# Kernel optimization log

Hardware: AMD Instinct MI355X
Metric: run time of the kernel (lower is better)

Reference implementation:

```python
import jax, jax.numpy as jnp
import numpy as np

EPS = 1e-5
INIT_PERSIST = 0.5

def _layernorm(x):
    mu = jnp.mean(x, axis=-1, keepdims=True)
    var = jnp.var(x, axis=-1, keepdims=True)
    return (x - mu) / jnp.sqrt(var + EPS)

def setup_inputs() -> dict:
    key = jax.random.key(0)
    k1, k2, k3, k4 = jax.random.split(key, 4)
    B, T, D, N = 8, 48, 512, 1024
    return {
        "x_seq": jax.random.normal(k1, (B, T, D), dtype=jnp.float32),
        "targets": jax.random.normal(k2, (B, T, D), dtype=jnp.float32),
        "E": jax.random.normal(k3, (D, N), dtype=jnp.float32) * 0.1,
        "Dy": jax.random.normal(k4, (N, D), dtype=jnp.float32) * 0.1,
        "mix_param": jnp.zeros((), dtype=jnp.float32),
    }

def reference(x_seq, targets, E, Dy, mix_param):
    B, T, D = x_seq.shape
    N = E.shape[1]
    alpha = jax.nn.sigmoid(mix_param)

    # initial states: persist = 0.5*I, transition = 0
    Gp0 = jnp.broadcast_to(jnp.eye(N, dtype=x_seq.dtype) * INIT_PERSIST, (B, N, N))
    Gt0 = jnp.zeros((B, N, N), dtype=x_seq.dtype)

    # target for step t's update is targets[:, t+1]; last step has no update
    tgt_next = jnp.concatenate([targets[:, 1:, :], jnp.zeros_like(targets[:, :1, :])], axis=1)
    do_upd = jnp.arange(T) < (T - 1)  # [T] bool

    xs = (jnp.swapaxes(x_seq, 0, 1), jnp.swapaxes(tgt_next, 0, 1), do_upd)

    def step(carry, inp):
        Gp, Gt = carry
        x_t, tn_t, upd = inp
        xn = jax.nn.relu(_layernorm(x_t @ E))          # [B, N]
        r_p = jnp.einsum("bn,bnm->bm", xn, Gp)
        r_t = jnp.einsum("bn,bnm->bm", xn, Gt)
        y = jax.nn.relu((alpha * r_p + (1.0 - alpha) * r_t) @ Dy)  # [B, D]
        tn = jax.nn.relu(_layernorm(tn_t @ E))          # [B, N]
        Gt_new = jnp.maximum(Gt, 0.5 * xn[:, :, None] * tn[:, None, :])
        Gp_new = jnp.maximum(Gp, 0.5 * xn[:, :, None] * xn[:, None, :])
        Gt = jnp.where(upd, Gt_new, Gt)
        Gp = jnp.where(upd, Gp_new, Gp)
        return (Gp, Gt), y

    _, ys = jax.lax.scan(step, (Gp0, Gt0), xs)
    return jnp.swapaxes(ys, 0, 1)  # [B, T, D]
```

## Files before the change

kernel.cpp:

```cpp
#include <hip/hip_runtime.h>
#include <math.h>

#define BB 8
#define TT 48
#define DD 512
#define NN 1024

__global__ __launch_bounds__(256) void k_gemm_z(const float* __restrict__ x,
                                                const float* __restrict__ tg,
                                                const float* __restrict__ E,
                                                float* __restrict__ z_x,
                                                float* __restrict__ z_t) {
    int rt = blockIdx.x, ct = blockIdx.y;
    int tid = threadIdx.x;
    int tr = tid >> 4;
    int tc = tid & 15;
    int row0 = rt * 32;
    int col0 = ct * 64;

    __shared__ float As[32][16];
    __shared__ float Es[16][64];

    int e2 = tid * 2;
    int sr = e2 >> 4;
    int sk0 = e2 & 15;
    int gr_s = row0 + sr;
    const float* srow;
    if (gr_s < BB * TT) {
        srow = x + (size_t)gr_s * DD;
    } else {
        int s = gr_s - BB * TT + 1;
        if (s > BB * TT - 1) s = BB * TT - 1;
        srow = tg + (size_t)s * DD;
    }

    int se = tid >> 4;
    int sc0 = (tid & 15) * 4;
    const float* erow = E + col0 + sc0;

    float4 acc0 = make_float4(0.f, 0.f, 0.f, 0.f);
    float4 acc1 = make_float4(0.f, 0.f, 0.f, 0.f);

    for (int d0 = 0; d0 < DD; d0 += 16) {
        float2 xv = *reinterpret_cast<const float2*>(srow + d0 + sk0);
        float4 ev = *reinterpret_cast<const float4*>(erow + (size_t)(d0 + se) * NN);
        __syncthreads();
        As[sr][sk0] = xv.x;
        As[sr][sk0 + 1] = xv.y;
        *reinterpret_cast<float4*>(&Es[se][sc0]) = ev;
        __syncthreads();
#pragma unroll
        for (int k = 0; k < 16; k++) {
            float a0 = As[tr][k];
            float a1 = As[tr + 16][k];
            float4 e = *reinterpret_cast<const float4*>(&Es[k][tc * 4]);
            acc0.x = fmaf(a0, e.x, acc0.x);
            acc0.y = fmaf(a0, e.y, acc0.y);
            acc0.z = fmaf(a0, e.z, acc0.z);
            acc0.w = fmaf(a0, e.w, acc0.w);
            acc1.x = fmaf(a1, e.x, acc1.x);
            acc1.y = fmaf(a1, e.y, acc1.y);
            acc1.z = fmaf(a1, e.z, acc1.z);
            acc1.w = fmaf(a1, e.w, acc1.w);
        }
    }

    int gr0 = row0 + tr, gr1 = row0 + tr + 16;
    int cbase = col0 + tc * 4;
    if (gr0 < BB * TT)
        *reinterpret_cast<float4*>(z_x + (size_t)gr0 * NN + cbase) = acc0;
    else
        *reinterpret_cast<float4*>(z_t + (size_t)(gr0 - BB * TT) * NN + cbase) = acc0;
    if (gr1 < BB * TT)
        *reinterpret_cast<float4*>(z_x + (size_t)gr1 * NN + cbase) = acc1;
    else
        *reinterpret_cast<float4*>(z_t + (size_t)(gr1 - BB * TT) * NN + cbase) = acc1;
}

__global__ __launch_bounds__(256) void k_ln(const float* __restrict__ z_x,
                                            const float* __restrict__ z_t,
                                            float* __restrict__ xn,
                                            float* __restrict__ tn) {
    int bt = blockIdx.x;
    int t = bt % TT;
    int tid = threadIdx.x;
    __shared__ float rs_[256], rq_[256];

    const float* src = z_x + (size_t)bt * NN;
    float v0 = src[tid], v1 = src[tid + 256], v2 = src[tid + 512], v3 = src[tid + 768];
    rs_[tid] = v0 + v1 + v2 + v3;
    rq_[tid] = v0 * v0 + v1 * v1 + v2 * v2 + v3 * v3;
    __syncthreads();
    for (int off = 128; off > 0; off >>= 1) {
        if (tid < off) { rs_[tid] += rs_[tid + off]; rq_[tid] += rq_[tid + off]; }
        __syncthreads();
    }
    float mu = rs_[0] * (1.f / NN);
    float var = rq_[0] * (1.f / NN) - mu * mu;
    float rstd = rsqrtf(var + 1e-5f);
    float* xrow = xn + (size_t)bt * NN;
    xrow[tid]       = fmaxf((v0 - mu) * rstd, 0.f);
    xrow[tid + 256] = fmaxf((v1 - mu) * rstd, 0.f);
    xrow[tid + 512] = fmaxf((v2 - mu) * rstd, 0.f);
    xrow[tid + 768] = fmaxf((v3 - mu) * rstd, 0.f);
    __syncthreads();

    float* trow = tn + (size_t)bt * NN;
    if (t < TT - 1) {
        const float* s2 = z_t + (size_t)bt * NN;
        float u0 = s2[tid], u1 = s2[tid + 256], u2 = s2[tid + 512], u3 = s2[tid + 768];
        rs_[tid] = u0 + u1 + u2 + u3;
        rq_[tid] = u0 * u0 + u1 * u1 + u2 * u2 + u3 * u3;
        __syncthreads();
        for (int off = 128; off > 0; off >>= 1) {
            if (tid < off) { rs_[tid] += rs_[tid + off]; rq_[tid] += rq_[tid + off]; }
            __syncthreads();
        }
        float mu2 = rs_[0] * (1.f / NN);
        float var2 = rq_[0] * (1.f / NN) - mu2 * mu2;
        float r2 = rsqrtf(var2 + 1e-5f);
        trow[tid]       = fmaxf((u0 - mu2) * r2, 0.f);
        trow[tid + 256] = fmaxf((u1 - mu2) * r2, 0.f);
        trow[tid + 512] = fmaxf((u2 - mu2) * r2, 0.f);
        trow[tid + 768] = fmaxf((u3 - mu2) * r2, 0.f);
    } else {
        trow[tid] = 0.f; trow[tid + 256] = 0.f; trow[tid + 512] = 0.f; trow[tid + 768] = 0.f;
    }
}


#define GI(n) float g##n = (state == 0 && nc == cc && (n) == lane) ? 0.5f : 0.f;
#define REP64(X) X(0) X(1) X(2) X(3) X(4) X(5) X(6) X(7) X(8) X(9) X(10) X(11) X(12) X(13) \
    X(14) X(15) X(16) X(17) X(18) X(19) X(20) X(21) X(22) X(23) X(24) X(25) X(26) X(27) \
    X(28) X(29) X(30) X(31) X(32) X(33) X(34) X(35) X(36) X(37) X(38) X(39) X(40) X(41) \
    X(42) X(43) X(44) X(45) X(46) X(47) X(48) X(49) X(50) X(51) X(52) X(53) X(54) X(55) \
    X(56) X(57) X(58) X(59) X(60) X(61) X(62) X(63)

#define GS(WE, n, A) { float wn_ = (WE); float tmp_;                             \
    asm("v_fmac_f32 %[a], %[w], %[g]\n\t"                                        \
        "v_mul_f32 %[t], %[w], %[m]\n\t"                                         \
        "v_max_f32 %[g], %[g], %[t]"                                             \
        : [a]"+v"(A), [g]"+v"(g##n), [t]"=&v"(tmp_)                              \
        : [w]"v"(wn_), [m]"v"(mh)); }

#define GQ(q, n0_, n1_, n2_, n3_) {                                              \
    float4 w4_ = *reinterpret_cast<const float4*>(&lw[(t << 6) + (q) * 4]);      \
    GS(w4_.x, n0_, a0) GS(w4_.y, n1_, a1) GS(w4_.z, n2_, a2) GS(w4_.w, n3_, a3) }

__global__ __launch_bounds__(256)
__attribute__((amdgpu_waves_per_eu(4, 4)))
void k_sweep(const float* __restrict__ xn,
             const float* __restrict__ tn,
             float* __restrict__ r_part) {
    int bid = blockIdx.x;
    int ccg = bid & 3, nc = (bid >> 2) & 15, b = (bid >> 6) & 7, state = bid >> 9;
    int tid = threadIdx.x;
    int lane = tid & 63;
    int wid = __builtin_amdgcn_readfirstlane(tid >> 6);
    int cc = ccg * 4 + wid;
    int n0 = nc * 64;
    int col = cc * 64 + lane;

    __shared__ float lw[TT * 64];

    REP64(GI)

    const float* wb  = xn + (size_t)b * TT * NN + n0;
    const float* mvb = (state ? tn : xn) + (size_t)b * TT * NN + col;
    float* rp = r_part + ((size_t)((state * 8 + b) * 16 + nc) * TT) * NN + col;

    for (int i = tid; i < TT * 64; i += 256)
        lw[i] = wb[(size_t)(i >> 6) * NN + (i & 63)];
    __syncthreads();

    float mv_cur = mvb[0];

#pragma unroll 1
    for (int t = 0; t < TT; t++) {
        int tn1 = (t + 1 < TT) ? t + 1 : TT - 1;
        float mv_nxt = mvb[(size_t)tn1 * NN];
        float sc = (t < TT - 1) ? 0.5f : 0.0f;
        float mh = mv_cur * sc;
        float a0 = 0.f, a1 = 0.f, a2 = 0.f, a3 = 0.f;
        GQ(0,  0,  1,  2,  3)
        GQ(1,  4,  5,  6,  7)
        GQ(2,  8,  9, 10, 11)
        GQ(3, 12, 13, 14, 15)
        GQ(4, 16, 17, 18, 19)
        GQ(5, 20, 21, 22, 23)
        GQ(6, 24, 25, 26, 27)
        GQ(7, 28, 29, 30, 31)
        GQ(8, 32, 33, 34, 35)
        GQ(9, 36, 37, 38, 39)
        GQ(10, 40, 41, 42, 43)
        GQ(11, 44, 45, 46, 47)
        GQ(12, 48, 49, 50, 51)
        GQ(13, 52, 53, 54, 55)
        GQ(14, 56, 57, 58, 59)
        GQ(15, 60, 61, 62, 63)
        rp[(size_t)t * NN] = (a0 + a1) + (a2 + a3);
        mv_cur = mv_nxt;
    }
}

__global__ __launch_bounds__(256) void k_mix(const float* __restrict__ r_part,
                                             const float* __restrict__ mixp,
                                             float* __restrict__ mix) {
    int bt = blockIdx.x;
    int b = bt / TT, t = bt % TT;
    int tid = threadIdx.x;
    int c0 = tid * 4;
    float alpha = 1.f / (1.f + expf(-mixp[0]));

    float spx = 0.f, spy = 0.f, spz = 0.f, spw = 0.f;
    float stx = 0.f, sty = 0.f, stz = 0.f, stw = 0.f;
#pragma unroll
    for (int nc = 0; nc < 16; nc++) {
        int bidp = (b * 16 + nc);
        int bidt = ((8 + b) * 16 + nc);
        float4 p = *reinterpret_cast<const float4*>(r_part + ((size_t)bidp * TT + t) * NN + c0);
        float4 q = *reinterpret_cast<const float4*>(r_part + ((size_t)bidt * TT + t) * NN + c0);
        spx += p.x; spy += p.y; spz += p.z; spw += p.w;
        stx += q.x; sty += q.y; stz += q.z; stw += q.w;
    }
    float4 m4;
    m4.x = alpha * spx + (1.f - alpha) * stx;
    m4.y = alpha * spy + (1.f - alpha) * sty;
    m4.z = alpha * spz + (1.f - alpha) * stz;
    m4.w = alpha * spw + (1.f - alpha) * stw;
    *reinterpret_cast<float4*>(mix + (size_t)bt * NN + c0) = m4;
}

__global__ __launch_bounds__(256) void k_y2(const float* __restrict__ mix,
                                            const float* __restrict__ Dy,
                                            float* __restrict__ out) {
    int ct = blockIdx.x;
    int rt = blockIdx.y;
    int tid = threadIdx.x;
    int row0 = rt * 16;
    int col0 = ct * 64;
    int r = tid >> 4;
    int tc = tid & 15;

    __shared__ float As[16][16];
    __shared__ float Ds[16][64];

    int sr = tid >> 4, sk = tid & 15;
    int se = tid >> 4, sc0 = (tid & 15) * 4;

    float4 acc = make_float4(0.f, 0.f, 0.f, 0.f);

    for (int m0 = 0; m0 < NN; m0 += 16) {
        float av = mix[(size_t)(row0 + sr) * NN + m0 + sk];
        float4 dv = *reinterpret_cast<const float4*>(Dy + (size_t)(m0 + se) * DD + col0 + sc0);
        __syncthreads();
        As[sr][sk] = av;
        *reinterpret_cast<float4*>(&Ds[se][sc0]) = dv;
        __syncthreads();
#pragma unroll
        for (int k = 0; k < 16; k++) {
            float a = As[r][k];
            float4 e = *reinterpret_cast<const float4*>(&Ds[k][tc * 4]);
            acc.x = fmaf(a, e.x, acc.x);
            acc.y = fmaf(a, e.y, acc.y);
            acc.z = fmaf(a, e.z, acc.z);
            acc.w = fmaf(a, e.w, acc.w);
        }
    }

    float4 o = make_float4(fmaxf(acc.x, 0.f), fmaxf(acc.y, 0.f),
                           fmaxf(acc.z, 0.f), fmaxf(acc.w, 0.f));
    *reinterpret_cast<float4*>(out + (size_t)(row0 + r) * DD + col0 + tc * 4) = o;
}

extern "C" void kernel_launch(void* const* d_in, const int* in_sizes, int n_in,
                              void* d_out, int out_size, void* d_ws, size_t ws_size,
                              hipStream_t stream) {
    const float* x    = (const float*)d_in[0];
    const float* tg   = (const float*)d_in[1];
    const float* E    = (const float*)d_in[2];
    const float* Dy   = (const float*)d_in[3];
    const float* mixp = (const float*)d_in[4];
    float* out = (float*)d_out;

    float* ws = (float*)d_ws;
    float* z_x    = ws;
    float* z_t    = z_x + (size_t)384 * 1024;
    float* xn     = z_t + (size_t)384 * 1024;
    float* tn     = xn + (size_t)384 * 1024;
    float* r_part = tn + (size_t)384 * 1024;
    float* mixbuf = r_part + (size_t)256 * 48 * 1024;

    k_gemm_z<<<dim3(24, 16), 256, 0, stream>>>(x, tg, E, z_x, z_t);
    k_ln<<<384, 256, 0, stream>>>(z_x, z_t, xn, tn);
    k_sweep<<<1024, 256, 0, stream>>>(xn, tn, r_part);
    k_mix<<<384, 256, 0, stream>>>(r_part, mixp, mixbuf);
    k_y2<<<dim3(8, 24), 256, 0, stream>>>(mixbuf, Dy, out);
}
```

Measured before the change: 137.6 us.

## Fuse persist and transition state sweeps into one block sharing LDS weights

Each sweep block now carries both the persist and transition state columns in registers (128 floats per thread) instead of launching separate blocks per state. The xn weight tile loaded into LDS and each float4 LDS read are reused for both states, halving LDS fills and reads and the block count. The cost is doubled register pressure, so occupancy is lowered to 2 waves per EU, which reduces latency hiding.

```diff
diff --git a/kernel.cpp b/kernel.cpp
--- a/kernel.cpp
+++ b/kernel.cpp
@@ -129,31 +129,40 @@
 }
 
 
-#define GI(n) float g##n = (state == 0 && nc == cc && (n) == lane) ? 0.5f : 0.f;
+#define GIP(n) float gp##n = (nc == cc && (n) == lane) ? 0.5f : 0.f;
+#define GIT(n) float gt##n = 0.f;
 #define REP64(X) X(0) X(1) X(2) X(3) X(4) X(5) X(6) X(7) X(8) X(9) X(10) X(11) X(12) X(13) \
     X(14) X(15) X(16) X(17) X(18) X(19) X(20) X(21) X(22) X(23) X(24) X(25) X(26) X(27) \
     X(28) X(29) X(30) X(31) X(32) X(33) X(34) X(35) X(36) X(37) X(38) X(39) X(40) X(41) \
     X(42) X(43) X(44) X(45) X(46) X(47) X(48) X(49) X(50) X(51) X(52) X(53) X(54) X(55) \
     X(56) X(57) X(58) X(59) X(60) X(61) X(62) X(63)
 
-#define GS(WE, n, A) { float wn_ = (WE); float tmp_;                             \
+#define GSP(WE, n, A) { float wn_ = (WE); float tmp_;                            \
     asm("v_fmac_f32 %[a], %[w], %[g]\n\t"                                        \
         "v_mul_f32 %[t], %[w], %[m]\n\t"                                         \
         "v_max_f32 %[g], %[g], %[t]"                                             \
-        : [a]"+v"(A), [g]"+v"(g##n), [t]"=&v"(tmp_)                              \
-        : [w]"v"(wn_), [m]"v"(mh)); }
+        : [a]"+v"(A), [g]"+v"(gp##n), [t]"=&v"(tmp_)                             \
+        : [w]"v"(wn_), [m]"v"(mhp)); }
+
+#define GST(WE, n, A) { float wn_ = (WE); float tmp_;                            \
+    asm("v_fmac_f32 %[a], %[w], %[g]\n\t"                                        \
+        "v_mul_f32 %[t], %[w], %[m]\n\t"                                         \
+        "v_max_f32 %[g], %[g], %[t]"                                             \
+        : [a]"+v"(A), [g]"+v"(gt##n), [t]"=&v"(tmp_)                             \
+        : [w]"v"(wn_), [m]"v"(mht)); }
 
 #define GQ(q, n0_, n1_, n2_, n3_) {                                              \
     float4 w4_ = *reinterpret_cast<const float4*>(&lw[(t << 6) + (q) * 4]);      \
-    GS(w4_.x, n0_, a0) GS(w4_.y, n1_, a1) GS(w4_.z, n2_, a2) GS(w4_.w, n3_, a3) }
+    GSP(w4_.x, n0_, ap0) GSP(w4_.y, n1_, ap1) GSP(w4_.z, n2_, ap2) GSP(w4_.w, n3_, ap3) \
+    GST(w4_.x, n0_, at0) GST(w4_.y, n1_, at1) GST(w4_.z, n2_, at2) GST(w4_.w, n3_, at3) }
 
 __global__ __launch_bounds__(256)
-__attribute__((amdgpu_waves_per_eu(4, 4)))
+__attribute__((amdgpu_waves_per_eu(2, 2)))
 void k_sweep(const float* __restrict__ xn,
              const float* __restrict__ tn,
              float* __restrict__ r_part) {
     int bid = blockIdx.x;
-    int ccg = bid & 3, nc = (bid >> 2) & 15, b = (bid >> 6) & 7, state = bid >> 9;
+    int ccg = bid & 3, nc = (bid >> 2) & 15, b = bid >> 6;
     int tid = threadIdx.x;
     int lane = tid & 63;
     int wid = __builtin_amdgcn_readfirstlane(tid >> 6);
@@ -163,25 +172,32 @@
 
     __shared__ float lw[TT * 64];
 
-    REP64(GI)
-
-    const float* wb  = xn + (size_t)b * TT * NN + n0;
-    const float* mvb = (state ? tn : xn) + (size_t)b * TT * NN + col;
-    float* rp = r_part + ((size_t)((state * 8 + b) * 16 + nc) * TT) * NN + col;
+    REP64(GIP)
+    REP64(GIT)
+
+    const float* wb   = xn + (size_t)b * TT * NN + n0;
+    const float* mvxb = xn + (size_t)b * TT * NN + col;
+    const float* mvtb = tn + (size_t)b * TT * NN + col;
+    float* rpp = r_part + ((size_t)(b * 16 + nc) * TT) * NN + col;
+    float* rpt = r_part + ((size_t)((8 + b) * 16 + nc) * TT) * NN + col;
 
     for (int i = tid; i < TT * 64; i += 256)
         lw[i] = wb[(size_t)(i >> 6) * NN + (i & 63)];
     __syncthreads();
 
-    float mv_cur = mvb[0];
+    float mvx_cur = mvxb[0];
+    float mvt_cur = mvtb[0];
 
 #pragma unroll 1
     for (int t = 0; t < TT; t++) {
         int tn1 = (t + 1 < TT) ? t + 1 : TT - 1;
-        float mv_nxt = mvb[(size_t)tn1 * NN];
+        float mvx_nxt = mvxb[(size_t)tn1 * NN];
+        float mvt_nxt = mvtb[(size_t)tn1 * NN];
         float sc = (t < TT - 1) ? 0.5f : 0.0f;
-        float mh = mv_cur * sc;
-        float a0 = 0.f, a1 = 0.f, a2 = 0.f, a3 = 0.f;
+        float mhp = mvx_cur * sc;
+        float mht = mvt_cur * sc;
+        float ap0 = 0.f, ap1 = 0.f, ap2 = 0.f, ap3 = 0.f;
+        float at0 = 0.f, at1 = 0.f, at2 = 0.f, at3 = 0.f;
         GQ(0,  0,  1,  2,  3)
         GQ(1,  4,  5,  6,  7)
         GQ(2,  8,  9, 10, 11)
@@ -198,8 +214,10 @@
         GQ(13, 52, 53, 54, 55)
         GQ(14, 56, 57, 58, 59)
         GQ(15, 60, 61, 62, 63)
-        rp[(size_t)t * NN] = (a0 + a1) + (a2 + a3);
-        mv_cur = mv_nxt;
+        rpp[(size_t)t * NN] = (ap0 + ap1) + (ap2 + ap3);
+        rpt[(size_t)t * NN] = (at0 + at1) + (at2 + at3);
+        mvx_cur = mvx_nxt;
+        mvt_cur = mvt_nxt;
     }
 }
 
@@ -293,7 +311,7 @@
 
     k_gemm_z<<<dim3(24, 16), 256, 0, stream>>>(x, tg, E, z_x, z_t);
     k_ln<<<384, 256, 0, stream>>>(z_x, z_t, xn, tn);
-    k_sweep<<<1024, 256, 0, stream>>>(xn, tn, r_part);
+    k_sweep<<<512, 256, 0, stream>>>(xn, tn, r_part);
     k_mix<<<384, 256, 0, stream>>>(r_part, mixp, mixbuf);
     k_y2<<<dim3(8, 24), 256, 0, stream>>>(mixbuf, Dy, out);
 }
```

Measured after the change: 143.2 us. 1.04x slower.
